# Performance work log

Measured on AMD Instinct MI355X. Metric: run time of the kernel, lower is better.

The kernel has to match this reference:

```python
import jax, jax.numpy as jnp
import numpy as np

B, T, C = 256, 1024, 128


def setup_inputs() -> dict:
    key = jax.random.key(0)
    k1, k2 = jax.random.split(key)
    potentials = jax.random.normal(k1, (B, T, C), dtype=jnp.float32)
    # glorot_uniform init for the [C, C] transition matrix
    limit = float(np.sqrt(6.0 / (C + C)))
    transitions = jax.random.uniform(k2, (C, C), minval=-limit, maxval=limit, dtype=jnp.float32)
    return {"potentials": potentials, "transitions": transitions}


def _viterbi_decode(potentials, transitions):
    """Equivalent of tfa.text.crf.crf_decode with full sequence lengths ('reg' mode).

    potentials: [B, T, C] unary scores; transitions: [C, C] (prev -> cur).
    Returns one-hot decoded tags [B, T, C] (the layer's inference output).
    """
    num_tags = potentials.shape[-1]
    pots_t = jnp.swapaxes(potentials, 0, 1)  # [T, B, C]
    alpha0 = pots_t[0]                        # [B, C]

    def fwd_step(alpha, pot):
        # max-plus DP step: scores[b, p, c] = alpha[b, p] + transitions[p, c]
        scores = alpha[:, :, None] + transitions[None, :, :]   # [B, C, C]
        bp = jnp.argmax(scores, axis=1).astype(jnp.int32)      # backpointers [B, C]
        alpha_new = jnp.max(scores, axis=1) + pot               # [B, C]
        return alpha_new, bp

    alpha_T, bps = jax.lax.scan(fwd_step, alpha0, pots_t[1:])   # bps: [T-1, B, C]
    last_tag = jnp.argmax(alpha_T, axis=-1).astype(jnp.int32)   # [B]

    def bwd_step(tag, bp):
        # tag at time t+1 -> best tag at time t via backpointers
        prev = jnp.take_along_axis(bp, tag[:, None], axis=1)[:, 0]
        return prev, prev

    _, prev_tags = jax.lax.scan(bwd_step, last_tag, bps, reverse=True)  # [T-1, B]
    tags = jnp.concatenate([prev_tags, last_tag[None, :]], axis=0)      # [T, B]
    tags = jnp.swapaxes(tags, 0, 1)                                      # [B, T]
    return jax.nn.one_hot(tags, num_tags, dtype=potentials.dtype)


def reference(potentials, transitions):
    return _viterbi_decode(potentials, transitions)
```

## Files before the change

kernel.cpp:

```cpp
#include <hip/hip_runtime.h>


typedef float f32x2 __attribute__((ext_vector_type(2)));
typedef unsigned int u32x4 __attribute__((ext_vector_type(4)));

constexpr int NB = 256;
constexpr int NT = 1024;
constexpr int NC = 128;

template <int CTRL>
__device__ __forceinline__ float fmax_dpp(float v) {
  int x = __builtin_amdgcn_update_dpp(__float_as_int(v), __float_as_int(v),
                                      CTRL, 0xF, 0xF, false);
  return fmaxf(v, __int_as_float(x));
}
__device__ __forceinline__ float wave_max_to_lane63(float m) {
  m = fmax_dpp<0x111>(m);
  m = fmax_dpp<0x112>(m);
  m = fmax_dpp<0x114>(m);
  m = fmax_dpp<0x118>(m);
  m = fmax_dpp<0x142>(m);
  m = fmax_dpp<0x143>(m);
  return m;
}

constexpr int ABUF = 192;

#define TREEA                                             \
  "v_pk_add_f32 v[32:33], v[48:49], v[64:65]\n\t"         \
  "v_pk_add_f32 v[34:35], v[50:51], v[66:67]\n\t"         \
  "v_pk_add_f32 v[36:37], v[52:53], v[68:69]\n\t"         \
  "v_pk_add_f32 v[38:39], v[54:55], v[70:71]\n\t"         \
  "v_pk_add_f32 v[40:41], v[56:57], v[72:73]\n\t"         \
  "v_pk_add_f32 v[42:43], v[58:59], v[74:75]\n\t"         \
  "v_pk_add_f32 v[44:45], v[60:61], v[76:77]\n\t"         \
  "v_pk_add_f32 v[46:47], v[62:63], v[78:79]\n\t"         \
  "v_max3_f32 v32, v32, v33, v34\n\t"                     \
  "v_max3_f32 v35, v35, v36, v37\n\t"                     \
  "v_max3_f32 v38, v38, v39, v40\n\t"                     \
  "v_max3_f32 v41, v41, v42, v43\n\t"                     \
  "v_max3_f32 v44, v44, v45, v46\n\t"                     \
  "v_max3_f32 v32, v32, v35, v38\n\t"                     \
  "v_max3_f32 v41, v41, v44, v47\n\t"                     \
  "v_max_f32 v32, v32, v41\n\t"

#define TREEB                                             \
  "v_pk_add_f32 v[96:97], v[48:49], v[80:81]\n\t"         \
  "v_pk_add_f32 v[98:99], v[50:51], v[82:83]\n\t"         \
  "v_pk_add_f32 v[100:101], v[52:53], v[84:85]\n\t"       \
  "v_pk_add_f32 v[102:103], v[54:55], v[86:87]\n\t"       \
  "v_pk_add_f32 v[104:105], v[56:57], v[88:89]\n\t"       \
  "v_pk_add_f32 v[106:107], v[58:59], v[90:91]\n\t"       \
  "v_pk_add_f32 v[108:109], v[60:61], v[92:93]\n\t"       \
  "v_pk_add_f32 v[110:111], v[62:63], v[94:95]\n\t"       \
  "v_max3_f32 v96, v96, v97, v98\n\t"                     \
  "v_max3_f32 v99, v99, v100, v101\n\t"                   \
  "v_max3_f32 v102, v102, v103, v104\n\t"                 \
  "v_max3_f32 v105, v105, v106, v107\n\t"                 \
  "v_max3_f32 v108, v108, v109, v110\n\t"                 \
  "v_max3_f32 v96, v96, v99, v102\n\t"                    \
  "v_max3_f32 v105, v105, v108, v111\n\t"                 \
  "v_max_f32 v96, v96, v105\n\t"

#define DPP2(CTL)                                                          \
  "v_max_f32_dpp v32, v32, v32 " CTL " row_mask:0xf bank_mask:0xf\n\t"     \
  "v_max_f32_dpp v96, v96, v96 " CTL " row_mask:0xf bank_mask:0xf\n\t"

#define STEP_S(RD, WR, PC, SOFF)                                           \
  "ds_read_b128 v[48:51], %[" RD "]\n\t"                                   \
  "ds_read_b128 v[52:55], %[" RD "] offset:16\n\t"                         \
  "ds_read_b128 v[56:59], %[" RD "] offset:48\n\t"                         \
  "ds_read_b128 v[60:63], %[" RD "] offset:64\n\t"                         \
  "s_waitcnt lgkmcnt(0)\n\t"                                               \
  TREEA                                                                    \
  TREEB                                                                    \
  "s_nop 1\n\t"                                                            \
  DPP2("quad_perm:[1,0,3,2]")                                              \
  "s_nop 0\n\t"                                                            \
  DPP2("quad_perm:[2,3,0,1]")                                              \
  "s_nop 0\n\t"                                                            \
  DPP2("row_half_mirror")                                                  \
  "s_nop 0\n\t"                                                            \
  "v_cndmask_b32 v41, v32, v96, %[selb0]\n\t"                              \
  "s_mov_b64 exec, %[wmask]\n\t"                                           \
  "v_add_f32 v40, v41, %[" PC "]\n\t"                                      \
  "ds_write_b32 %[" WR "], v40\n\t"                                        \
  "global_store_dword %[qoff], v41, %[sout] offset:" SOFF "\n\t"           \
  "s_mov_b64 exec, -1\n\t"                                                 \
  "s_waitcnt lgkmcnt(0)\n\t"                                               \
  "s_barrier\n\t"

#define LDT(R, B, O) "global_load_dword v" R ", %[" B "], %[strans] offset:" O "\n\t"

__global__ __launch_bounds__(512, 2)
void crf_fwd(const float* __restrict__ pot, const float* __restrict__ trans,
             float* __restrict__ out) {
  __shared__ __align__(16) float alpha[2 * ABUF];

  const int tid = threadIdx.x;
  const int b = blockIdx.x;
  const int w = tid >> 6;
  const int l = tid & 63;
  const int g = l >> 3;
  const int i = l & 7;
  const int G = w * 8 + g;
  const bool wr = (l & 7) < 2;
  const int cw = 16 * w + 2 * g + (l & 1);
  const int widx = 12 * (cw >> 3) + (cw & 7);

  const float* potb = pot + (size_t)b * NT * NC;
  float* outb = out + (size_t)b * NT * NC;

  unsigned rda = (unsigned)(size_t)(alpha + 24 * i);
  unsigned rdb = (unsigned)(size_t)(alpha + ABUF + 24 * i);
  unsigned wra = (unsigned)(size_t)(alpha + widx);
  unsigned wrb = (unsigned)(size_t)(alpha + ABUF + widx);

  unsigned toff  = (unsigned)((16 * i * NC + 2 * G) * 4);
  unsigned toff2 = toff + 4096;
  unsigned qoff = (unsigned)((1 * NC + cw) * 4);
  unsigned poff = ((unsigned)b * (NT * NC) + 5 * NC + cw) * 4u;
  unsigned long long strans = (unsigned long long)(size_t)trans;
  unsigned long long sout = (unsigned long long)(size_t)outb;
  unsigned long long pbase = (unsigned long long)(size_t)pot;
  u32x4 srd;
  srd.x = (unsigned)pbase;
  srd.y = (unsigned)(pbase >> 32) & 0xFFFFu;
  srd.z = (unsigned)(NB * NT * NC) * 4u;
  srd.w = 0x00020000u;
  unsigned long long selb0 = 0xAAAAAAAAAAAAAAAAull;
  unsigned long long wmask = 0x0303030303030303ull;
  int cnt = 254;

  float pc0 = potb[1 * NC + cw], pc1 = potb[2 * NC + cw];
  float pc2 = potb[3 * NC + cw], pc3 = potb[4 * NC + cw];
  float pn0 = 0.f, pn1 = 0.f, pn2 = 0.f, pn3 = 0.f;

  if (wr) {
    alpha[widx] = potb[cw];
    outb[cw] = 0.0f;
  }
  __syncthreads();

  asm volatile(
      LDT("64","toff","0")     LDT("65","toff","512")
      LDT("66","toff","1024")  LDT("67","toff","1536")
      LDT("68","toff","2048")  LDT("69","toff","2560")
      LDT("70","toff","3072")  LDT("71","toff","3584")
      LDT("72","toff2","0")    LDT("73","toff2","512")
      LDT("74","toff2","1024") LDT("75","toff2","1536")
      LDT("76","toff2","2048") LDT("77","toff2","2560")
      LDT("78","toff2","3072") LDT("79","toff2","3584")
      LDT("80","toff","4")     LDT("81","toff","516")
      LDT("82","toff","1028")  LDT("83","toff","1540")
      LDT("84","toff","2052")  LDT("85","toff","2564")
      LDT("86","toff","3076")  LDT("87","toff","3588")
      LDT("88","toff2","4")    LDT("89","toff2","516")
      LDT("90","toff2","1028") LDT("91","toff2","1540")
      LDT("92","toff2","2052") LDT("93","toff2","2564")
      LDT("94","toff2","3076") LDT("95","toff2","3588")
      "s_waitcnt vmcnt(0)\n\t"
      "buffer_load_dword %[pn0], %[poff], %[srd], 0 offen\n\t"
      "buffer_load_dword %[pn1], %[poff], %[srd], 0 offen offset:512\n\t"
      "buffer_load_dword %[pn2], %[poff], %[srd], 0 offen offset:1024\n\t"
      "buffer_load_dword %[pn3], %[poff], %[srd], 0 offen offset:1536\n\t"
      "L_crfmain_%=:\n\t"
      STEP_S("rda", "wrb", "pc0", "0")
      STEP_S("rdb", "wra", "pc1", "512")
      STEP_S("rda", "wrb", "pc2", "1024")
      STEP_S("rdb", "wra", "pc3", "1536")
      "s_waitcnt vmcnt(4)\n\t"
      "v_mov_b32 %[pc0], %[pn0]\n\t"
      "v_mov_b32 %[pc1], %[pn1]\n\t"
      "v_mov_b32 %[pc2], %[pn2]\n\t"
      "v_mov_b32 %[pc3], %[pn3]\n\t"
      "v_add_u32 %[poff], 0x800, %[poff]\n\t"
      "v_add_u32 %[qoff], 0x800, %[qoff]\n\t"
      "buffer_load_dword %[pn0], %[poff], %[srd], 0 offen\n\t"
      "buffer_load_dword %[pn1], %[poff], %[srd], 0 offen offset:512\n\t"
      "buffer_load_dword %[pn2], %[poff], %[srd], 0 offen offset:1024\n\t"
      "buffer_load_dword %[pn3], %[poff], %[srd], 0 offen offset:1536\n\t"
      "s_sub_u32 %[cnt], %[cnt], 1\n\t"
      "s_cmp_lg_u32 %[cnt], 0\n\t"
      "s_cbranch_scc1 L_crfmain_%=\n\t"
      STEP_S("rda", "wrb", "pc0", "0")
      STEP_S("rdb", "wra", "pc1", "512")
      STEP_S("rda", "wrb", "pc2", "1024")
      STEP_S("rdb", "wra", "pc3", "1536")
      "s_waitcnt vmcnt(4)\n\t"
      "v_mov_b32 %[pc0], %[pn0]\n\t"
      "v_mov_b32 %[pc1], %[pn1]\n\t"
      "v_mov_b32 %[pc2], %[pn2]\n\t"
      "v_add_u32 %[qoff], 0x800, %[qoff]\n\t"
      STEP_S("rda", "wrb", "pc0", "0")
      STEP_S("rdb", "wra", "pc1", "512")
      STEP_S("rda", "wrb", "pc2", "1024")
      : [pc0] "+v"(pc0), [pc1] "+v"(pc1), [pc2] "+v"(pc2), [pc3] "+v"(pc3),
        [pn0] "+v"(pn0), [pn1] "+v"(pn1), [pn2] "+v"(pn2), [pn3] "+v"(pn3),
        [qoff] "+v"(qoff), [poff] "+v"(poff), [cnt] "+s"(cnt)
      : [toff] "v"(toff), [toff2] "v"(toff2),
        [rda] "v"(rda), [rdb] "v"(rdb), [wra] "v"(wra), [wrb] "v"(wrb),
        [strans] "s"(strans), [sout] "s"(sout), [srd] "s"(srd),
        [selb0] "s"(selb0), [wmask] "s"(wmask)
      : "memory", "scc",
        "v32", "v33", "v34", "v35", "v36", "v37", "v38", "v39",
        "v40", "v41", "v42", "v43", "v44", "v45", "v46", "v47",
        "v48", "v49", "v50", "v51", "v52", "v53", "v54", "v55",
        "v56", "v57", "v58", "v59", "v60", "v61", "v62", "v63",
        "v64", "v65", "v66", "v67", "v68", "v69", "v70", "v71",
        "v72", "v73", "v74", "v75", "v76", "v77", "v78", "v79",
        "v80", "v81", "v82", "v83", "v84", "v85", "v86", "v87",
        "v88", "v89", "v90", "v91", "v92", "v93", "v94", "v95",
        "v96", "v97", "v98", "v99", "v100", "v101", "v102", "v103",
        "v104", "v105", "v106", "v107", "v108", "v109", "v110", "v111");
}


__global__ __launch_bounds__(256)
void crf_bwd(const float* __restrict__ pot, const float* __restrict__ trans,
             float* __restrict__ out) {
  extern __shared__ float tTf[];
  const int tid = threadIdx.x;
  const int b = blockIdx.x;
  const float* potb = pot + (size_t)b * NT * NC;
  float* outb = out + (size_t)b * NT * NC;

  {
    const int rr = tid >> 1;
    const int h = tid & 1;
    const float4* src = (const float4*)(trans + rr * NC + h * 64);
    const int lo = rr & 63, hb = rr >> 6;
    #pragma unroll
    for (int j = 0; j < 16; ++j) {
      float4 q = src[j];
      int cb = h * 64 + 4 * j;
      tTf[(cb + 0) * 128 + lo * 2 + hb] = q.x;
      tTf[(cb + 1) * 128 + lo * 2 + hb] = q.y;
      tTf[(cb + 2) * 128 + lo * 2 + hb] = q.z;
      tTf[(cb + 3) * 128 + lo * 2 + hb] = q.w;
    }
  }
  __syncthreads();
  if (tid >= 64) return;
  const int l = tid;
  const f32x2* tTp = (const f32x2*)tTf;

  float qlo_t = outb[(NT - 1) * NC + l];
  float qhi_t = outb[(NT - 1) * NC + 64 + l];
  float alo_t = qlo_t + potb[(NT - 1) * NC + l];
  float ahi_t = qhi_t + potb[(NT - 1) * NC + 64 + l];
  float m0 = wave_max_to_lane63(fmaxf(alo_t, ahi_t));
  float M0 = __int_as_float(__builtin_amdgcn_readlane(__float_as_int(m0), 63));
  unsigned long long bl = __ballot(alo_t == M0);
  unsigned long long bh = __ballot(ahi_t == M0);
  int tag = bl ? (__ffsll((long long)bl) - 1)
               : (64 + __ffsll((long long)bh) - 1);

  float cqlo[8], cqhi[8], calo[8], cahi[8];
  float nqlo[8], nqhi[8], nplo[8], nphi[8];
  #pragma unroll
  for (int j = 0; j < 8; ++j) {
    int rw = NT - 2 - j;
    cqlo[j] = outb[rw * NC + l];
    cqhi[j] = outb[rw * NC + 64 + l];
    calo[j] = cqlo[j] + potb[rw * NC + l];
    cahi[j] = cqhi[j] + potb[rw * NC + 64 + l];
  }

  for (int g = 0; g < 128; ++g) {
    #pragma unroll
    for (int j = 0; j < 8; ++j) {
      int rw = NT - 10 - 8 * g - j;
      if (rw < 0) rw = 0;
      nqlo[j] = outb[rw * NC + l];
      nqhi[j] = outb[rw * NC + 64 + l];
      nplo[j] = potb[rw * NC + l];
      nphi[j] = potb[rw * NC + 64 + l];
    }
    #pragma unroll
    for (int j = 0; j < 8; ++j) {
      int t = NT - 1 - 8 * g - j;
      if (t >= 1) {
        outb[t * NC + l]      = (l == tag) ? 1.0f : 0.0f;
        outb[t * NC + 64 + l] = (64 + l == tag) ? 1.0f : 0.0f;
        int Mlo = __builtin_amdgcn_readlane(__float_as_int(qlo_t), tag & 63);
        int Mhi = __builtin_amdgcn_readlane(__float_as_int(qhi_t), tag & 63);
        float M = __int_as_float((tag < 64) ? Mlo : Mhi);
        f32x2 tt = tTp[tag * 64 + l];
        float vlo = calo[j] + tt.x;
        float vhi = cahi[j] + tt.y;
        unsigned long long el = __ballot(vlo == M);
        unsigned long long eh = __ballot(vhi == M);
        tag = el ? (__ffsll((long long)el) - 1)
                 : (64 + __ffsll((long long)eh) - 1);
        qlo_t = cqlo[j];
        qhi_t = cqhi[j];
      }
    }
    #pragma unroll
    for (int j = 0; j < 8; ++j) {
      cqlo[j] = nqlo[j]; cqhi[j] = nqhi[j];
      calo[j] = nqlo[j] + nplo[j];
      cahi[j] = nqhi[j] + nphi[j];
    }
  }
  outb[l]      = (l == tag) ? 1.0f : 0.0f;
  outb[64 + l] = (64 + l == tag) ? 1.0f : 0.0f;
}


extern "C" void kernel_launch(void* const* d_in, const int* in_sizes, int n_in,
                              void* d_out, int out_size, void* d_ws, size_t ws_size,
                              hipStream_t stream) {
  const float* pot   = (const float*)d_in[0];
  const float* trans = (const float*)d_in[1];
  float* out = (float*)d_out;

  hipFuncSetAttribute((const void*)crf_bwd,
                      hipFuncAttributeMaxDynamicSharedMemorySize, NC * NC * 4);

  crf_fwd<<<NB, 512, 0, stream>>>(pot, trans, out);
  crf_bwd<<<NB, 256, NC * NC * 4, stream>>>(pot, trans, out);
}
```

Before: 418.9 us.

## Fuse forward and backtrack kernels and split LDS wait in DP step

Merges the forward max-plus kernel and the backtracking kernel into one launch. The backtrack now runs in the same block after a barrier, with the transposed transition matrix staged in dynamic LDS by all 512 threads. It also splits the LDS read wait so the first half of the add/max tree starts while the last two reads are still in flight. Costs: a second launch and its gap are removed, but 64KB of LDS per block may lower occupancy, and launch_bounds drops the min-blocks hint.

Result: no change. 414.2 us, median of 2 (-1.1%).

```diff
diff --git a/kernel.cpp b/kernel.cpp
--- a/kernel.cpp
+++ b/kernel.cpp
@@ -26,42 +26,6 @@
 
 constexpr int ABUF = 192;
 
-#define TREEA                                             \
-  "v_pk_add_f32 v[32:33], v[48:49], v[64:65]\n\t"         \
-  "v_pk_add_f32 v[34:35], v[50:51], v[66:67]\n\t"         \
-  "v_pk_add_f32 v[36:37], v[52:53], v[68:69]\n\t"         \
-  "v_pk_add_f32 v[38:39], v[54:55], v[70:71]\n\t"         \
-  "v_pk_add_f32 v[40:41], v[56:57], v[72:73]\n\t"         \
-  "v_pk_add_f32 v[42:43], v[58:59], v[74:75]\n\t"         \
-  "v_pk_add_f32 v[44:45], v[60:61], v[76:77]\n\t"         \
-  "v_pk_add_f32 v[46:47], v[62:63], v[78:79]\n\t"         \
-  "v_max3_f32 v32, v32, v33, v34\n\t"                     \
-  "v_max3_f32 v35, v35, v36, v37\n\t"                     \
-  "v_max3_f32 v38, v38, v39, v40\n\t"                     \
-  "v_max3_f32 v41, v41, v42, v43\n\t"                     \
-  "v_max3_f32 v44, v44, v45, v46\n\t"                     \
-  "v_max3_f32 v32, v32, v35, v38\n\t"                     \
-  "v_max3_f32 v41, v41, v44, v47\n\t"                     \
-  "v_max_f32 v32, v32, v41\n\t"
-
-#define TREEB                                             \
-  "v_pk_add_f32 v[96:97], v[48:49], v[80:81]\n\t"         \
-  "v_pk_add_f32 v[98:99], v[50:51], v[82:83]\n\t"         \
-  "v_pk_add_f32 v[100:101], v[52:53], v[84:85]\n\t"       \
-  "v_pk_add_f32 v[102:103], v[54:55], v[86:87]\n\t"       \
-  "v_pk_add_f32 v[104:105], v[56:57], v[88:89]\n\t"       \
-  "v_pk_add_f32 v[106:107], v[58:59], v[90:91]\n\t"       \
-  "v_pk_add_f32 v[108:109], v[60:61], v[92:93]\n\t"       \
-  "v_pk_add_f32 v[110:111], v[62:63], v[94:95]\n\t"       \
-  "v_max3_f32 v96, v96, v97, v98\n\t"                     \
-  "v_max3_f32 v99, v99, v100, v101\n\t"                   \
-  "v_max3_f32 v102, v102, v103, v104\n\t"                 \
-  "v_max3_f32 v105, v105, v106, v107\n\t"                 \
-  "v_max3_f32 v108, v108, v109, v110\n\t"                 \
-  "v_max3_f32 v96, v96, v99, v102\n\t"                    \
-  "v_max3_f32 v105, v105, v108, v111\n\t"                 \
-  "v_max_f32 v96, v96, v105\n\t"
-
 #define DPP2(CTL)                                                          \
   "v_max_f32_dpp v32, v32, v32 " CTL " row_mask:0xf bank_mask:0xf\n\t"     \
   "v_max_f32_dpp v96, v96, v96 " CTL " row_mask:0xf bank_mask:0xf\n\t"
@@ -71,9 +35,40 @@
   "ds_read_b128 v[52:55], %[" RD "] offset:16\n\t"                         \
   "ds_read_b128 v[56:59], %[" RD "] offset:48\n\t"                         \
   "ds_read_b128 v[60:63], %[" RD "] offset:64\n\t"                         \
+  "s_waitcnt lgkmcnt(2)\n\t"                                               \
+  "v_pk_add_f32 v[32:33], v[48:49], v[64:65]\n\t"                          \
+  "v_pk_add_f32 v[96:97], v[48:49], v[80:81]\n\t"                          \
+  "v_pk_add_f32 v[34:35], v[50:51], v[66:67]\n\t"                          \
+  "v_pk_add_f32 v[98:99], v[50:51], v[82:83]\n\t"                          \
+  "v_pk_add_f32 v[36:37], v[52:53], v[68:69]\n\t"                          \
+  "v_pk_add_f32 v[100:101], v[52:53], v[84:85]\n\t"                        \
+  "v_pk_add_f32 v[38:39], v[54:55], v[70:71]\n\t"                          \
+  "v_pk_add_f32 v[102:103], v[54:55], v[86:87]\n\t"                        \
+  "v_max3_f32 v32, v32, v33, v34\n\t"                                      \
+  "v_max3_f32 v96, v96, v97, v98\n\t"                                      \
+  "v_max3_f32 v35, v35, v36, v37\n\t"                                      \
+  "v_max3_f32 v99, v99, v100, v101\n\t"                                    \
   "s_waitcnt lgkmcnt(0)\n\t"                                               \
-  TREEA                                                                    \
-  TREEB                                                                    \
+  "v_pk_add_f32 v[40:41], v[56:57], v[72:73]\n\t"                          \
+  "v_pk_add_f32 v[104:105], v[56:57], v[88:89]\n\t"                        \
+  "v_pk_add_f32 v[42:43], v[58:59], v[74:75]\n\t"                          \
+  "v_pk_add_f32 v[106:107], v[58:59], v[90:91]\n\t"                        \
+  "v_pk_add_f32 v[44:45], v[60:61], v[76:77]\n\t"                          \
+  "v_pk_add_f32 v[108:109], v[60:61], v[92:93]\n\t"                        \
+  "v_pk_add_f32 v[46:47], v[62:63], v[78:79]\n\t"                          \
+  "v_pk_add_f32 v[110:111], v[62:63], v[94:95]\n\t"                        \
+  "v_max3_f32 v38, v38, v39, v40\n\t"                                      \
+  "v_max3_f32 v102, v102, v103, v104\n\t"                                  \
+  "v_max3_f32 v41, v41, v42, v43\n\t"                                      \
+  "v_max3_f32 v105, v105, v106, v107\n\t"                                  \
+  "v_max3_f32 v44, v44, v45, v46\n\t"                                      \
+  "v_max3_f32 v108, v108, v109, v110\n\t"                                  \
+  "v_max3_f32 v32, v32, v35, v38\n\t"                                      \
+  "v_max3_f32 v96, v96, v99, v102\n\t"                                     \
+  "v_max3_f32 v41, v41, v44, v47\n\t"                                      \
+  "v_max3_f32 v105, v105, v108, v111\n\t"                                  \
+  "v_max_f32 v32, v32, v41\n\t"                                            \
+  "v_max_f32 v96, v96, v105\n\t"                                           \
   "s_nop 1\n\t"                                                            \
   DPP2("quad_perm:[1,0,3,2]")                                              \
   "s_nop 0\n\t"                                                            \
@@ -92,10 +87,12 @@
 
 #define LDT(R, B, O) "global_load_dword v" R ", %[" B "], %[strans] offset:" O "\n\t"
 
-__global__ __launch_bounds__(512, 2)
-void crf_fwd(const float* __restrict__ pot, const float* __restrict__ trans,
-             float* __restrict__ out) {
-  __shared__ __align__(16) float alpha[2 * ABUF];
+__global__ __launch_bounds__(512)
+void crf_fused(const float* __restrict__ pot, const float* __restrict__ trans,
+               float* __restrict__ out) {
+  extern __shared__ __align__(16) float smem[];
+  float* alpha = smem;
+  float* tTf = smem + 2 * ABUF;
 
   const int tid = threadIdx.x;
   const int b = blockIdx.x;
@@ -195,6 +192,7 @@
       STEP_S("rda", "wrb", "pc0", "0")
       STEP_S("rdb", "wra", "pc1", "512")
       STEP_S("rda", "wrb", "pc2", "1024")
+      "s_waitcnt vmcnt(0)\n\t"
       : [pc0] "+v"(pc0), [pc1] "+v"(pc1), [pc2] "+v"(pc2), [pc3] "+v"(pc3),
         [pn0] "+v"(pn0), [pn1] "+v"(pn1), [pn2] "+v"(pn2), [pn3] "+v"(pn3),
         [qoff] "+v"(qoff), [poff] "+v"(poff), [cnt] "+s"(cnt)
@@ -213,36 +211,25 @@
         "v88", "v89", "v90", "v91", "v92", "v93", "v94", "v95",
         "v96", "v97", "v98", "v99", "v100", "v101", "v102", "v103",
         "v104", "v105", "v106", "v107", "v108", "v109", "v110", "v111");
-}
-
-
-__global__ __launch_bounds__(256)
-void crf_bwd(const float* __restrict__ pot, const float* __restrict__ trans,
-             float* __restrict__ out) {
-  extern __shared__ float tTf[];
-  const int tid = threadIdx.x;
-  const int b = blockIdx.x;
-  const float* potb = pot + (size_t)b * NT * NC;
-  float* outb = out + (size_t)b * NT * NC;
-
+
+  __syncthreads();
   {
-    const int rr = tid >> 1;
-    const int h = tid & 1;
-    const float4* src = (const float4*)(trans + rr * NC + h * 64);
+    const int rr = tid >> 2;
+    const int q4 = tid & 3;
+    const float4* src = (const float4*)(trans + rr * NC + q4 * 32);
     const int lo = rr & 63, hb = rr >> 6;
     #pragma unroll
-    for (int j = 0; j < 16; ++j) {
-      float4 q = src[j];
-      int cb = h * 64 + 4 * j;
-      tTf[(cb + 0) * 128 + lo * 2 + hb] = q.x;
-      tTf[(cb + 1) * 128 + lo * 2 + hb] = q.y;
-      tTf[(cb + 2) * 128 + lo * 2 + hb] = q.z;
-      tTf[(cb + 3) * 128 + lo * 2 + hb] = q.w;
+    for (int j = 0; j < 8; ++j) {
+      float4 qv = src[j];
+      int cb = q4 * 32 + 4 * j;
+      tTf[(cb + 0) * 128 + lo * 2 + hb] = qv.x;
+      tTf[(cb + 1) * 128 + lo * 2 + hb] = qv.y;
+      tTf[(cb + 2) * 128 + lo * 2 + hb] = qv.z;
+      tTf[(cb + 3) * 128 + lo * 2 + hb] = qv.w;
     }
   }
   __syncthreads();
   if (tid >= 64) return;
-  const int l = tid;
   const f32x2* tTp = (const f32x2*)tTf;
 
   float qlo_t = outb[(NT - 1) * NC + l];
@@ -267,10 +254,10 @@
     cahi[j] = cqhi[j] + potb[rw * NC + 64 + l];
   }
 
-  for (int g = 0; g < 128; ++g) {
+  for (int g2 = 0; g2 < 128; ++g2) {
     #pragma unroll
     for (int j = 0; j < 8; ++j) {
-      int rw = NT - 10 - 8 * g - j;
+      int rw = NT - 10 - 8 * g2 - j;
       if (rw < 0) rw = 0;
       nqlo[j] = outb[rw * NC + l];
       nqhi[j] = outb[rw * NC + 64 + l];
@@ -279,7 +266,7 @@
     }
     #pragma unroll
     for (int j = 0; j < 8; ++j) {
-      int t = NT - 1 - 8 * g - j;
+      int t = NT - 1 - 8 * g2 - j;
       if (t >= 1) {
         outb[t * NC + l]      = (l == tag) ? 1.0f : 0.0f;
         outb[t * NC + 64 + l] = (64 + l == tag) ? 1.0f : 0.0f;
@@ -316,9 +303,9 @@
   const float* trans = (const float*)d_in[1];
   float* out = (float*)d_out;
 
-  hipFuncSetAttribute((const void*)crf_bwd,
-                      hipFuncAttributeMaxDynamicSharedMemorySize, NC * NC * 4);
-
-  crf_fwd<<<NB, 512, 0, stream>>>(pot, trans, out);
-  crf_bwd<<<NB, 256, NC * NC * 4, stream>>>(pot, trans, out);
+  constexpr int SMEM = (2 * ABUF + NC * NC) * 4;
+  hipFuncSetAttribute((const void*)crf_fused,
+                      hipFuncAttributeMaxDynamicSharedMemorySize, SMEM);
+
+  crf_fused<<<NB, 512, SMEM, stream>>>(pot, trans, out);
 }
```
